# Kernel optimization log

Measured on AMD Instinct MI355X. Metric: run time of the kernel, lower is better.

## Reference

```python
import jax, jax.numpy as jnp
import numpy as np

B, N, F_IN = 32, 512, 64
HEADS = (8, 8)
HIDS = (64, 64)
EDGE_P = 0.05  # graph density
NEG_SLOPE = 0.2
NEG_INF = -1e20


def setup_inputs() -> dict:
    key = jax.random.key(0)
    ks = jax.random.split(key, 8)
    x = jax.random.normal(ks[0], (B, N, F_IN), dtype=jnp.float32)
    adj = (jax.random.uniform(ks[1], (B, N, N)) < EDGE_P).astype(jnp.float32)
    adj = jnp.maximum(adj, adj.transpose(0, 2, 1))  # symmetric adjacency
    # mask = (batch, row): every (b, n) pair gets the masked softmax
    b_idx = jnp.repeat(jnp.arange(B, dtype=jnp.int32), N)   # [B*N]
    r_idx = jnp.tile(jnp.arange(N, dtype=jnp.int32), B)     # [B*N]
    # layer 0: f_in=64 -> f_out=64, H=8 ; layer 1: f_in=64*8=512 -> f_out=64, H=8
    W0 = jax.random.normal(ks[2], (F_IN, HIDS[0]), dtype=jnp.float32) / jnp.sqrt(jnp.float32(F_IN))
    a_src0 = jax.random.normal(ks[3], (HIDS[0], HEADS[0]), dtype=jnp.float32) / jnp.sqrt(jnp.float32(HIDS[0]))
    a_dst0 = jax.random.normal(ks[4], (HIDS[0], HEADS[0]), dtype=jnp.float32) / jnp.sqrt(jnp.float32(HIDS[0]))
    f_in1 = HIDS[0] * HEADS[0]
    W1 = jax.random.normal(ks[5], (f_in1, HIDS[1]), dtype=jnp.float32) / jnp.sqrt(jnp.float32(f_in1))
    a_src1 = jax.random.normal(ks[6], (HIDS[1], HEADS[1]), dtype=jnp.float32) / jnp.sqrt(jnp.float32(HIDS[1]))
    a_dst1 = jax.random.normal(ks[7], (HIDS[1], HEADS[1]), dtype=jnp.float32) / jnp.sqrt(jnp.float32(HIDS[1]))
    return dict(x=x, adj=adj, b_idx=b_idx, r_idx=r_idx,
                W0=W0, a_src0=a_src0, a_dst0=a_dst0,
                W1=W1, a_src1=a_src1, a_dst1=a_dst1)


def _gat_layer(x, adj, b_idx, r_idx, W, a_src, a_dst):
    # x: [B,N,f_in], adj: [B,N,N] (diag already set), W: [f_in,F], a_*: [F,H]
    hp = x @ W                                        # [B,N,F]
    s = jnp.einsum('bnf,fh->bhn', hp, a_src)          # attn_src
    d = jnp.einsum('bnf,fh->bhn', hp, a_dst)          # attn_dst
    attn = s[:, :, :, None] + d[:, :, None, :]        # [B,H,N,N]
    attn = jnp.where(attn >= 0, attn, NEG_SLOPE * attn)  # leaky_relu(0.2)
    attn = jnp.where(adj[:, None, :, :] == 0, 0.0, attn)  # masked_fill(adj==0, 0)
    rows = attn[b_idx, :, r_idx, :]                   # [K,H,N]
    rows = jnp.where(rows == 0.0, NEG_INF, rows)
    rows = jax.nn.softmax(rows, axis=-1)
    attn = attn.at[b_idx, :, r_idx, :].set(rows)
    return jnp.einsum('bhij,bjf->bhif', attn, hp)     # [B,H,N,F]


def reference(x, adj, b_idx, r_idx, W0, a_src0, a_dst0, W1, a_src1, a_dst1):
    Bn, Nn = x.shape[:2]
    # torch mutates adj in place: adj[batch,row,row] = 1 (self loops)
    adj = adj.at[b_idx, r_idx, r_idx].set(1.0)
    o = _gat_layer(x, adj, b_idx, r_idx, W0, a_src0, a_dst0)      # [B,H,N,F0]
    x1 = jax.nn.elu(o.transpose(0, 2, 1, 3).reshape(Bn, Nn, -1))  # [B,N,H*F0]
    o2 = _gat_layer(x1, adj, b_idx, r_idx, W1, a_src1, a_dst1)    # [B,H,N,F1]
    return o2.mean(axis=1)                                        # [B,N,F1]
```

## Files before the change

### kernel.cpp

```cpp
#include <hip/hip_runtime.h>
#include <hip/hip_bf16.h>
#include <math.h>

#define BB 32
#define NN 512

typedef _Float16 f16x8 __attribute__((ext_vector_type(8)));
typedef __fp16  fp16x2 __attribute__((ext_vector_type(2)));
typedef float f32x4 __attribute__((ext_vector_type(4)));

#define MFMA16(a, b, c) __builtin_amdgcn_mfma_f32_16x16x32_f16(a, b, c, 0, 0, 0)

union AF { f16x8 v; unsigned int u[4]; };

__global__ __launch_bounds__(256) void k_wt_prep(
    const float* __restrict__ W0, _Float16* __restrict__ W0T,
    const float* __restrict__ W1, _Float16* __restrict__ W1T)
{
    int id = blockIdx.x * 256 + threadIdx.x;
    const float* W; _Float16* WT; int KT, task;
    if (id < 512) { W = W0; WT = W0T; KT = 64;  task = id; }
    else          { W = W1; WT = W1T; KT = 512; task = id - 512; }
    int n = task & 63, gabs = task >> 6;
    int c = gabs >> 3, g = gabs & 7;
    f16x8 hv;
#pragma unroll
    for (int e = 0; e < 8; ++e)
        hv[e] = (_Float16)W[(size_t)(gabs * 8 + e) * 64 + n];
    *(f16x8*)(WT + (size_t)n * KT + c * 64 + (g ^ (n & 7)) * 8) = hv;
}

__global__ __launch_bounds__(256) void k_maxd(
    const float* __restrict__ dTg, float* __restrict__ maxd)
{
    __shared__ float sm[4];
    int bh = blockIdx.x;
    int t = threadIdx.x, lane = t & 63, w = t >> 6;
    const float* p = dTg + (size_t)bh * NN;
    float m = fmaxf(p[t], p[t + 256]);
#pragma unroll
    for (int off = 32; off; off >>= 1) m = fmaxf(m, __shfl_xor(m, off));
    if (lane == 0) sm[w] = m;
    __syncthreads();
    if (t == 0) maxd[bh] = fmaxf(fmaxf(sm[0], sm[1]), fmaxf(sm[2], sm[3]));
}

static __device__ __forceinline__ void epi_sd_hpt(
    const float* ctile, const float* asd_f, int row0, int t,
    float* __restrict__ s, float* __restrict__ dTg, _Float16* __restrict__ hpT)
{
    int b = row0 >> 9, jb = row0 & 511;
    if (t < 128) {
        int rr = t >> 3, h = t & 7;
        float sv = 0.f, dv = 0.f;
#pragma unroll
        for (int f = 0; f < 64; ++f) {
            float hv = ctile[rr * 66 + f];
            sv = fmaf(hv, asd_f[f * 8 + h], sv);
            dv = fmaf(hv, asd_f[512 + f * 8 + h], dv);
        }
        s[((size_t)b * NN + jb + rr) * 8 + h] = sv;
        dTg[((size_t)b * 8 + h) * NN + jb + rr] = dv;
    } else {
        int t2 = t - 128;
        int f = t2 >> 1, jl = (t2 & 1) * 8;
        f16x8 hv;
#pragma unroll
        for (int e = 0; e < 8; ++e)
            hv[e] = (_Float16)ctile[(jl + e) * 66 + f];
        *(f16x8*)(hpT + ((size_t)b * 64 + f) * NN + jb + jl) = hv;
    }
}

__global__ __launch_bounds__(256) void k_gemm0(
    const float* __restrict__ x, const _Float16* __restrict__ W0T,
    const float* __restrict__ a_src, const float* __restrict__ a_dst,
    float* __restrict__ s, float* __restrict__ dTg, _Float16* __restrict__ hpT)
{
    __shared__ float ctile[16 * 66];
    __shared__ float asd_f[1024];
    int t = threadIdx.x, row0 = blockIdx.x * 16;
    int lane = t & 63, w = t >> 6, cn = lane & 15, rq = lane >> 4;

    ((float4*)asd_f)[t] = (t < 128) ? ((const float4*)a_src)[t]
                                    : ((const float4*)a_dst)[t - 128];
    f32x4 acc;
#pragma unroll
    for (int e = 0; e < 4; ++e) acc[e] = 0.f;
#pragma unroll
    for (int ks = 0; ks < 2; ++ks) {
        const float* xp = x + (size_t)(row0 + cn) * 64 + ks * 32 + rq * 8;
        float4 x0 = *(const float4*)xp, x1 = *(const float4*)(xp + 4);
        f16x8 ah = {(_Float16)x0.x, (_Float16)x0.y, (_Float16)x0.z, (_Float16)x0.w,
                    (_Float16)x1.x, (_Float16)x1.y, (_Float16)x1.z, (_Float16)x1.w};
        int nn = w * 16 + cn;
        f16x8 bh = *(const f16x8*)(W0T + (size_t)nn * 64 + (((ks * 4 + rq) ^ (nn & 7)) * 8));
        acc = MFMA16(ah, bh, acc);
    }
#pragma unroll
    for (int r = 0; r < 4; ++r)
        ctile[(rq * 4 + r) * 66 + w * 16 + cn] = acc[r];
    __syncthreads();
    epi_sd_hpt(ctile, asd_f, row0, t, s, dTg, hpT);
}

template<int MODE>
__global__ __launch_bounds__(256, 4) void k_attn_fused(
    const float* __restrict__ adj, const float* __restrict__ s,
    const float* __restrict__ dTg, const float* __restrict__ maxd,
    const _Float16* __restrict__ hpT,
    const _Float16* __restrict__ W1T,
    const float* __restrict__ a_src, const float* __restrict__ a_dst,
    float* __restrict__ s_out, float* __restrict__ dTg_out,
    _Float16* __restrict__ hpT_out, float* __restrict__ o_f)
{
    __shared__ __align__(16) char smem[32768];
    _Float16* hT = (_Float16*)smem;

    int blk = blockIdx.x;
    int vb = ((blk & 7) << 7) | (blk >> 3);
    int b = vb >> 5, i0 = (vb & 31) << 4;
    int row0 = vb * 16;
    int t = threadIdx.x, lane = t & 63, w = t >> 6;
    int cn = lane & 15, rq = lane >> 4;
    int h0 = 2 * w, h1 = h0 + 1;
    int myrow = i0 + cn;

    float sv0 = s[((size_t)b * NN + myrow) * 8 + h0];
    float sv1 = s[((size_t)b * NN + myrow) * 8 + h1];
    float M0 = fmaxf(sv0 + maxd[b * 8 + h0], 0.f);
    float M1 = fmaxf(sv1 + maxd[b * 8 + h1], 0.f);

    const float* arow = adj + ((size_t)b * NN + myrow) * NN;
    const float* dg0 = dTg + ((size_t)b * 8 + h0) * NN;
    const float* dg1 = dTg + ((size_t)b * 8 + h1) * NN;
    const _Float16* hb = hpT + (size_t)b * 64 * NN;

    int f0 = t >> 3, g0 = t & 7;
    int f1 = f0 + 32;
    int sw = ((g0 ^ (f0 & 7)) * 8);
    int sw0 = f0 * 64 + sw, sw1 = f1 * 64 + sw;

    f16x8 ones;
#pragma unroll
    for (int e = 0; e < 8; ++e) ones[e] = (_Float16)1.0f;

    f32x4 acc[2][4], accrs[2];
#pragma unroll
    for (int hh = 0; hh < 2; ++hh) {
#pragma unroll
        for (int e = 0; e < 4; ++e) accrs[hh][e] = 0.f;
#pragma unroll
        for (int ft = 0; ft < 4; ++ft)
#pragma unroll
            for (int e = 0; e < 4; ++e) acc[hh][ft][e] = 0.f;
    }

    uint4 rH0 = *(const uint4*)(hb + (size_t)f0 * 512 + g0 * 8);
    uint4 rH1 = *(const uint4*)(hb + (size_t)f1 * 512 + g0 * 8);

    for (int jcx = 0; jcx < 8; ++jcx) {
        int jc = jcx * 64;
        float aa[2][8], dd0[2][8], dd1[2][8];
#pragma unroll
        for (int ks = 0; ks < 2; ++ks) {
            int j0 = jc + ks * 32 + rq * 8;
            *(float4*)&aa[ks][0]  = *(const float4*)(arow + j0);
            *(float4*)&aa[ks][4]  = *(const float4*)(arow + j0 + 4);
            *(float4*)&dd0[ks][0] = *(const float4*)(dg0 + j0);
            *(float4*)&dd0[ks][4] = *(const float4*)(dg0 + j0 + 4);
            *(float4*)&dd1[ks][0] = *(const float4*)(dg1 + j0);
            *(float4*)&dd1[ks][4] = *(const float4*)(dg1 + j0 + 4);
        }
        *(uint4*)&hT[sw0] = rH0;
        *(uint4*)&hT[sw1] = rH1;
        __syncthreads();
        if (jcx < 7) {
            rH0 = *(const uint4*)(hb + (size_t)f0 * 512 + jc + 64 + g0 * 8);
            rH1 = *(const uint4*)(hb + (size_t)f1 * 512 + jc + 64 + g0 * 8);
        }
#pragma unroll
        for (int ks = 0; ks < 2; ++ks) {
            int j0 = jc + ks * 32 + rq * 8;
            int rel = myrow - j0;
            AF aA, aB;
#pragma unroll
            for (int e = 0; e < 8; e += 2) {
                float pA[2], pB[2];
#pragma unroll
                for (int q = 0; q < 2; ++q) {
                    int ee = e + q;
                    bool con = (aa[ks][ee] != 0.f) || (ee == rel);
                    float e0 = sv0 + dd0[ks][ee];
                    float l0 = fmaxf(e0, 0.2f * e0);
                    float p0 = __expf(l0 - M0);
                    pA[q] = (con && l0 != 0.f) ? p0 : 0.f;
                    float e1 = sv1 + dd1[ks][ee];
                    float l1 = fmaxf(e1, 0.2f * e1);
                    float p1 = __expf(l1 - M1);
                    pB[q] = (con && l1 != 0.f) ? p1 : 0.f;
                }
                fp16x2 ka = __builtin_amdgcn_cvt_pkrtz(pA[0], pA[1]);
                fp16x2 kb = __builtin_amdgcn_cvt_pkrtz(pB[0], pB[1]);
                aA.u[e >> 1] = __builtin_bit_cast(unsigned int, ka);
                aB.u[e >> 1] = __builtin_bit_cast(unsigned int, kb);
            }
            accrs[0] = MFMA16(aA.v, ones, accrs[0]);
            accrs[1] = MFMA16(aB.v, ones, accrs[1]);
#pragma unroll
            for (int ft = 0; ft < 4; ++ft) {
                int f = ft * 16 + cn;
                f16x8 bh = *(const f16x8*)&hT[f * 64 + (((ks * 4 + rq) ^ (f & 7)) * 8)];
                acc[0][ft] = MFMA16(aA.v, bh, acc[0][ft]);
                acc[1][ft] = MFMA16(aB.v, bh, acc[1][ft]);
            }
        }
        __syncthreads();
    }

    float invr[2][4];
#pragma unroll
    for (int hh = 0; hh < 2; ++hh)
#pragma unroll
        for (int r = 0; r < 4; ++r) invr[hh][r] = 1.0f / accrs[hh][r];

    if (MODE == 0) {
        _Float16* x1all = (_Float16*)(smem + 8192);
#pragma unroll
        for (int hh = 0; hh < 2; ++hh) {
            int h = h0 + hh;
#pragma unroll
            for (int ft = 0; ft < 4; ++ft)
#pragma unroll
                for (int r = 0; r < 4; ++r) {
                    int il = rq * 4 + r;
                    float v = acc[hh][ft][r] * invr[hh][r];
                    v = v > 0.f ? v : __expf(v) - 1.f;
                    int f = ft * 16 + cn;
                    x1all[h * 1024 + il * 64 + (((f >> 3) ^ (il & 7)) * 8) + (f & 7)] =
                        (_Float16)v;
                }
        }

        _Float16* Bst[2] = { (_Float16*)smem, (_Float16*)(smem + 24576) };
        {
#pragma unroll
            for (int u = 0; u < 2; ++u) {
                int idx = t + u * 256;
                *(uint4*)&Bst[0][idx * 8] =
                    *(const uint4*)(W1T + (size_t)(idx >> 3) * 512 + (idx & 7) * 8);
            }
        }
        f32x4 g1;
#pragma unroll
        for (int e = 0; e < 4; ++e) g1[e] = 0.f;
        uint4 rB0, rB1;
        for (int kc = 0; kc < 8; ++kc) {
            int cur = kc & 1;
            if (kc < 7) {
                rB0 = *(const uint4*)(W1T + (size_t)(t >> 3) * 512 + (kc + 1) * 64 + (t & 7) * 8);
                rB1 = *(const uint4*)(W1T + (size_t)((t + 256) >> 3) * 512 + (kc + 1) * 64 + (t & 7) * 8);
            }
            __syncthreads();
#pragma unroll
            for (int ks = 0; ks < 2; ++ks) {
                int pa = (((ks * 4 + rq) ^ (cn & 7)) * 8);
                f16x8 ah = *(const f16x8*)&x1all[kc * 1024 + cn * 64 + pa];
                int nn = w * 16 + cn;
                f16x8 bh = *(const f16x8*)&Bst[cur][nn * 64 + (((ks * 4 + rq) ^ (nn & 7)) * 8)];
                g1 = MFMA16(ah, bh, g1);
            }
            if (kc < 7) {
                *(uint4*)&Bst[cur ^ 1][t * 8] = rB0;
                *(uint4*)&Bst[cur ^ 1][(t + 256) * 8] = rB1;
            }
        }
        __syncthreads();
        float* ctile = (float*)(smem + 8192);
        float* asd_f = (float*)(smem + 16384);
#pragma unroll
        for (int r = 0; r < 4; ++r)
            ctile[(rq * 4 + r) * 66 + w * 16 + cn] = g1[r];
        ((float4*)asd_f)[t] = (t < 128) ? ((const float4*)a_src)[t]
                                        : ((const float4*)a_dst)[t - 128];
        __syncthreads();
        epi_sd_hpt(ctile, asd_f, row0, t, s_out, dTg_out, hpT_out);
    } else {
        float* red = (float*)smem;
#pragma unroll
        for (int ft = 0; ft < 4; ++ft)
#pragma unroll
            for (int r = 0; r < 4; ++r) {
                int il = rq * 4 + r;
                float v = acc[0][ft][r] * invr[0][r]
                        + acc[1][ft][r] * invr[1][r];
                red[(w * 16 + il) * 64 + ft * 16 + cn] = v;
            }
        __syncthreads();
#pragma unroll
        for (int u = 0; u < 4; ++u) {
            int idx = t + u * 256;
            int il = idx >> 6, f = idx & 63;
            float sum = red[il * 64 + f] + red[(16 + il) * 64 + f]
                      + red[(32 + il) * 64 + f] + red[(48 + il) * 64 + f];
            o_f[((size_t)b * NN + i0 + il) * 64 + f] = sum * 0.125f;
        }
    }
}

extern "C" void kernel_launch(void* const* d_in, const int* in_sizes, int n_in,
                              void* d_out, int out_size, void* d_ws, size_t ws_size,
                              hipStream_t stream) {
    const float* x      = (const float*)d_in[0];
    const float* adj    = (const float*)d_in[1];
    const float* W0     = (const float*)d_in[4];
    const float* a_src0 = (const float*)d_in[5];
    const float* a_dst0 = (const float*)d_in[6];
    const float* W1     = (const float*)d_in[7];
    const float* a_src1 = (const float*)d_in[8];
    const float* a_dst1 = (const float*)d_in[9];
    float* out = (float*)d_out;

    float* ws = (float*)d_ws;
    const size_t R = (size_t)BB * NN;
    float* s0    = ws;
    float* dTg0  = s0 + R * 8;
    float* s1    = dTg0 + (size_t)BB * 8 * NN;
    float* dTg1  = s1 + R * 8;
    float* maxd0 = dTg1 + (size_t)BB * 8 * NN;
    float* maxd1 = maxd0 + 256;
    _Float16* hp0T = (_Float16*)(maxd1 + 256);
    _Float16* hp1T = hp0T + (size_t)BB * 64 * NN;
    _Float16* W0T  = hp1T + (size_t)BB * 64 * NN;
    _Float16* W1T  = W0T + (size_t)64 * 64;

    k_wt_prep<<<18, 256, 0, stream>>>(W0, W0T, W1, W1T);
    k_gemm0<<<1024, 256, 0, stream>>>(x, W0T, a_src0, a_dst0, s0, dTg0, hp0T);
    k_maxd<<<256, 256, 0, stream>>>(dTg0, maxd0);
    k_attn_fused<0><<<1024, 256, 0, stream>>>(adj, s0, dTg0, maxd0, hp0T,
                                              W1T, a_src1, a_dst1,
                                              s1, dTg1, hp1T, nullptr);
    k_maxd<<<256, 256, 0, stream>>>(dTg1, maxd1);
    k_attn_fused<1><<<1024, 256, 0, stream>>>(adj, s1, dTg1, maxd1, hp1T,
                                              nullptr, nullptr, nullptr,
                                              nullptr, nullptr, nullptr, out);
}
```

Before: 164.4 us.

## Bitpack adjacency, factor softmax exponentials, and stage tiles via direct global-to-LDS loads

The adjacency matrix is packed into 64-bit ballot masks inside the first GEMM kernel, so the two attention passes read 1 bit instead of 4 bytes per edge. The exponential is factored into per-row and per-column terms: exp(d - max) and exp(0.2*(d - max)) are precomputed per column in the max kernel, leaving only a multiply per edge. The hpT and W1T tiles are double-buffered in LDS using global_load_lds, which removes the register round trip. The cost is extra E/Eb arrays that are read per element, and possible precision differences from the factored exponent.

After: 187.8 us. 14.2% more time.

```diff
diff --git a/kernel.cpp b/kernel.cpp
--- a/kernel.cpp
+++ b/kernel.cpp
@@ -12,6 +12,12 @@
 #define MFMA16(a, b, c) __builtin_amdgcn_mfma_f32_16x16x32_f16(a, b, c, 0, 0, 0)
 
 union AF { f16x8 v; unsigned int u[4]; };
+
+__device__ __forceinline__ void gload_lds16(const void* g, void* l) {
+    __builtin_amdgcn_global_load_lds(
+        (const __attribute__((address_space(1))) unsigned int*)g,
+        (__attribute__((address_space(3))) unsigned int*)l, 16, 0, 0);
+}
 
 __global__ __launch_bounds__(256) void k_wt_prep(
     const float* __restrict__ W0, _Float16* __restrict__ W0T,
@@ -31,18 +37,27 @@
 }
 
 __global__ __launch_bounds__(256) void k_maxd(
-    const float* __restrict__ dTg, float* __restrict__ maxd)
+    const float* __restrict__ dTg, float* __restrict__ maxd,
+    float* __restrict__ E, float* __restrict__ Eb)
 {
     __shared__ float sm[4];
     int bh = blockIdx.x;
     int t = threadIdx.x, lane = t & 63, w = t >> 6;
     const float* p = dTg + (size_t)bh * NN;
-    float m = fmaxf(p[t], p[t + 256]);
+    float d0 = p[t], d1 = p[t + 256];
+    float m = fmaxf(d0, d1);
 #pragma unroll
     for (int off = 32; off; off >>= 1) m = fmaxf(m, __shfl_xor(m, off));
     if (lane == 0) sm[w] = m;
     __syncthreads();
-    if (t == 0) maxd[bh] = fmaxf(fmaxf(sm[0], sm[1]), fmaxf(sm[2], sm[3]));
+    float mx = fmaxf(fmaxf(sm[0], sm[1]), fmaxf(sm[2], sm[3]));
+    if (t == 0) maxd[bh] = mx;
+    float* Ep  = E  + (size_t)bh * NN;
+    float* Ebp = Eb + (size_t)bh * NN;
+    Ep[t]        = __expf(d0 - mx);
+    Ep[t + 256]  = __expf(d1 - mx);
+    Ebp[t]       = __expf(0.2f * (d0 - mx));
+    Ebp[t + 256] = __expf(0.2f * (d1 - mx));
 }
 
 static __device__ __forceinline__ void epi_sd_hpt(
@@ -75,6 +90,7 @@
 __global__ __launch_bounds__(256) void k_gemm0(
     const float* __restrict__ x, const _Float16* __restrict__ W0T,
     const float* __restrict__ a_src, const float* __restrict__ a_dst,
+    const float* __restrict__ adj, unsigned long long* __restrict__ adjb,
     float* __restrict__ s, float* __restrict__ dTg, _Float16* __restrict__ hpT)
 {
     __shared__ float ctile[16 * 66];
@@ -102,12 +118,26 @@
         ctile[(rq * 4 + r) * 66 + w * 16 + cn] = acc[r];
     __syncthreads();
     epi_sd_hpt(ctile, asd_f, row0, t, s, dTg, hpT);
+
+#pragma unroll
+    for (int rl = 0; rl < 4; ++rl) {
+        int gi = row0 + w * 4 + rl;
+        int i = gi & (NN - 1);
+        const float* ap = adj + (size_t)gi * NN;
+#pragma unroll
+        for (int jc8 = 0; jc8 < 8; ++jc8) {
+            float v = ap[jc8 * 64 + lane];
+            unsigned long long m = __ballot((v != 0.f) || (jc8 * 64 + lane == i));
+            if (lane == 0) adjb[(size_t)gi * 8 + jc8] = m;
+        }
+    }
 }
 
 template<int MODE>
 __global__ __launch_bounds__(256, 4) void k_attn_fused(
-    const float* __restrict__ adj, const float* __restrict__ s,
+    const unsigned long long* __restrict__ adjb, const float* __restrict__ s,
     const float* __restrict__ dTg, const float* __restrict__ maxd,
+    const float* __restrict__ E, const float* __restrict__ Eb,
     const _Float16* __restrict__ hpT,
     const _Float16* __restrict__ W1T,
     const float* __restrict__ a_src, const float* __restrict__ a_dst,
@@ -115,7 +145,8 @@
     _Float16* __restrict__ hpT_out, float* __restrict__ o_f)
 {
     __shared__ __align__(16) char smem[32768];
-    _Float16* hT = (_Float16*)smem;
+    _Float16* hTd0 = (_Float16*)smem;
+    _Float16* hTd1 = (_Float16*)(smem + 8192);
 
     int blk = blockIdx.x;
     int vb = ((blk & 7) << 7) | (blk >> 3);
@@ -126,20 +157,33 @@
     int h0 = 2 * w, h1 = h0 + 1;
     int myrow = i0 + cn;
 
+    const _Float16* hb = hpT + (size_t)b * 64 * NN;
+
+    int f0 = t >> 3, g0 = t & 7;
+    const _Float16* src0 = hb + (size_t)f0 * NN + ((g0 ^ (f0 & 7)) * 8);
+    const _Float16* src1 = hb + (size_t)(f0 + 32) * NN + ((g0 ^ (f0 & 7)) * 8);
+    {
+        _Float16* db = hTd0 + (w << 9);
+        gload_lds16(src0, db);
+        gload_lds16(src1, db + 2048);
+    }
+
     float sv0 = s[((size_t)b * NN + myrow) * 8 + h0];
     float sv1 = s[((size_t)b * NN + myrow) * 8 + h1];
-    float M0 = fmaxf(sv0 + maxd[b * 8 + h0], 0.f);
-    float M1 = fmaxf(sv1 + maxd[b * 8 + h1], 0.f);
-
-    const float* arow = adj + ((size_t)b * NN + myrow) * NN;
-    const float* dg0 = dTg + ((size_t)b * 8 + h0) * NN;
-    const float* dg1 = dTg + ((size_t)b * 8 + h1) * NN;
-    const _Float16* hb = hpT + (size_t)b * 64 * NN;
-
-    int f0 = t >> 3, g0 = t & 7;
-    int f1 = f0 + 32;
-    int sw = ((g0 ^ (f0 & 7)) * 8);
-    int sw0 = f0 * 64 + sw, sw1 = f1 * 64 + sw;
+    float md0 = maxd[b * 8 + h0], md1 = maxd[b * 8 + h1];
+    float M0 = fmaxf(sv0 + md0, 0.f);
+    float M1 = fmaxf(sv1 + md1, 0.f);
+    float c00 = __expf(sv0 + md0 - M0), cb0 = __expf(0.2f * (sv0 + md0) - M0);
+    float c01 = __expf(sv1 + md1 - M1), cb1 = __expf(0.2f * (sv1 + md1) - M1);
+
+    const float* dg0  = dTg + ((size_t)b * 8 + h0) * NN;
+    const float* dg1  = dTg + ((size_t)b * 8 + h1) * NN;
+    const float* Er0  = E   + ((size_t)b * 8 + h0) * NN;
+    const float* Er1  = E   + ((size_t)b * 8 + h1) * NN;
+    const float* Ebr0 = Eb  + ((size_t)b * 8 + h0) * NN;
+    const float* Ebr1 = Eb  + ((size_t)b * 8 + h1) * NN;
+    const unsigned long long* abr = adjb + ((size_t)b * NN + myrow) * 8;
+    int rq8 = rq * 8;
 
     f16x8 ones;
 #pragma unroll
@@ -156,33 +200,37 @@
             for (int e = 0; e < 4; ++e) acc[hh][ft][e] = 0.f;
     }
 
-    uint4 rH0 = *(const uint4*)(hb + (size_t)f0 * 512 + g0 * 8);
-    uint4 rH1 = *(const uint4*)(hb + (size_t)f1 * 512 + g0 * 8);
-
+    unsigned long long mb = abr[0];
+    __syncthreads();
+
+#pragma unroll 2
     for (int jcx = 0; jcx < 8; ++jcx) {
         int jc = jcx * 64;
-        float aa[2][8], dd0[2][8], dd1[2][8];
+        const _Float16* hTc = (jcx & 1) ? hTd1 : hTd0;
+        if (jcx < 7) {
+            _Float16* db = ((jcx & 1) ? hTd0 : hTd1) + (w << 9);
+            gload_lds16(src0 + jc + 64, db);
+            gload_lds16(src1 + jc + 64, db + 2048);
+        }
+        unsigned long long mbn = (jcx < 7) ? abr[jcx + 1] : 0ull;
+        unsigned int ml = (unsigned int)mb, mhh = (unsigned int)(mb >> 32);
 #pragma unroll
         for (int ks = 0; ks < 2; ++ks) {
-            int j0 = jc + ks * 32 + rq * 8;
-            *(float4*)&aa[ks][0]  = *(const float4*)(arow + j0);
-            *(float4*)&aa[ks][4]  = *(const float4*)(arow + j0 + 4);
-            *(float4*)&dd0[ks][0] = *(const float4*)(dg0 + j0);
-            *(float4*)&dd0[ks][4] = *(const float4*)(dg0 + j0 + 4);
-            *(float4*)&dd1[ks][0] = *(const float4*)(dg1 + j0);
-            *(float4*)&dd1[ks][4] = *(const float4*)(dg1 + j0 + 4);
-        }
-        *(uint4*)&hT[sw0] = rH0;
-        *(uint4*)&hT[sw1] = rH1;
-        __syncthreads();
-        if (jcx < 7) {
-            rH0 = *(const uint4*)(hb + (size_t)f0 * 512 + jc + 64 + g0 * 8);
-            rH1 = *(const uint4*)(hb + (size_t)f1 * 512 + jc + 64 + g0 * 8);
-        }
-#pragma unroll
-        for (int ks = 0; ks < 2; ++ks) {
-            int j0 = jc + ks * 32 + rq * 8;
-            int rel = myrow - j0;
+            int j0 = jc + ks * 32 + rq8;
+            unsigned int mby = ((ks ? mhh : ml) >> rq8) & 0xffu;
+            float dd0[8], dd1[8], Ev0[8], Ev1[8], Eb0v[8], Eb1v[8];
+            *(float4*)&dd0[0]  = *(const float4*)(dg0 + j0);
+            *(float4*)&dd0[4]  = *(const float4*)(dg0 + j0 + 4);
+            *(float4*)&dd1[0]  = *(const float4*)(dg1 + j0);
+            *(float4*)&dd1[4]  = *(const float4*)(dg1 + j0 + 4);
+            *(float4*)&Ev0[0]  = *(const float4*)(Er0 + j0);
+            *(float4*)&Ev0[4]  = *(const float4*)(Er0 + j0 + 4);
+            *(float4*)&Ev1[0]  = *(const float4*)(Er1 + j0);
+            *(float4*)&Ev1[4]  = *(const float4*)(Er1 + j0 + 4);
+            *(float4*)&Eb0v[0] = *(const float4*)(Ebr0 + j0);
+            *(float4*)&Eb0v[4] = *(const float4*)(Ebr0 + j0 + 4);
+            *(float4*)&Eb1v[0] = *(const float4*)(Ebr1 + j0);
+            *(float4*)&Eb1v[4] = *(const float4*)(Ebr1 + j0 + 4);
             AF aA, aB;
 #pragma unroll
             for (int e = 0; e < 8; e += 2) {
@@ -190,15 +238,13 @@
 #pragma unroll
                 for (int q = 0; q < 2; ++q) {
                     int ee = e + q;
-                    bool con = (aa[ks][ee] != 0.f) || (ee == rel);
-                    float e0 = sv0 + dd0[ks][ee];
-                    float l0 = fmaxf(e0, 0.2f * e0);
-                    float p0 = __expf(l0 - M0);
-                    pA[q] = (con && l0 != 0.f) ? p0 : 0.f;
-                    float e1 = sv1 + dd1[ks][ee];
-                    float l1 = fmaxf(e1, 0.2f * e1);
-                    float p1 = __expf(l1 - M1);
-                    pB[q] = (con && l1 != 0.f) ? p1 : 0.f;
+                    bool con = (mby >> ee) & 1u;
+                    float e0 = sv0 + dd0[ee];
+                    float p0 = (e0 >= 0.f) ? c00 * Ev0[ee] : cb0 * Eb0v[ee];
+                    pA[q] = (con && e0 != 0.f) ? p0 : 0.f;
+                    float e1 = sv1 + dd1[ee];
+                    float p1 = (e1 >= 0.f) ? c01 * Ev1[ee] : cb1 * Eb1v[ee];
+                    pB[q] = (con && e1 != 0.f) ? p1 : 0.f;
                 }
                 fp16x2 ka = __builtin_amdgcn_cvt_pkrtz(pA[0], pA[1]);
                 fp16x2 kb = __builtin_amdgcn_cvt_pkrtz(pB[0], pB[1]);
@@ -210,11 +256,12 @@
 #pragma unroll
             for (int ft = 0; ft < 4; ++ft) {
                 int f = ft * 16 + cn;
-                f16x8 bh = *(const f16x8*)&hT[f * 64 + (((ks * 4 + rq) ^ (f & 7)) * 8)];
+                f16x8 bh = *(const f16x8*)&hTc[f * 64 + (((ks * 4 + rq) ^ (f & 7)) * 8)];
                 acc[0][ft] = MFMA16(aA.v, bh, acc[0][ft]);
                 acc[1][ft] = MFMA16(aB.v, bh, acc[1][ft]);
             }
         }
+        mb = mbn;
         __syncthreads();
     }
 
@@ -225,7 +272,15 @@
         for (int r = 0; r < 4; ++r) invr[hh][r] = 1.0f / accrs[hh][r];
 
     if (MODE == 0) {
-        _Float16* x1all = (_Float16*)(smem + 8192);
+        _Float16* Bst0 = (_Float16*)smem;
+        _Float16* Bst1 = (_Float16*)(smem + 8192);
+        const _Float16* wsrc = W1T + (size_t)(t >> 3) * 512 + ((t & 7) * 8);
+        {
+            _Float16* db = Bst0 + (w << 9);
+            gload_lds16(wsrc, db);
+            gload_lds16(wsrc + 32 * 512, db + 2048);
+        }
+        _Float16* x1all = (_Float16*)(smem + 16384);
 #pragma unroll
         for (int hh = 0; hh < 2; ++hh) {
             int h = h0 + hh;
@@ -241,43 +296,29 @@
                         (_Float16)v;
                 }
         }
-
-        _Float16* Bst[2] = { (_Float16*)smem, (_Float16*)(smem + 24576) };
-        {
-#pragma unroll
-            for (int u = 0; u < 2; ++u) {
-                int idx = t + u * 256;
-                *(uint4*)&Bst[0][idx * 8] =
-                    *(const uint4*)(W1T + (size_t)(idx >> 3) * 512 + (idx & 7) * 8);
-            }
-        }
+        __syncthreads();
         f32x4 g1;
 #pragma unroll
         for (int e = 0; e < 4; ++e) g1[e] = 0.f;
-        uint4 rB0, rB1;
         for (int kc = 0; kc < 8; ++kc) {
-            int cur = kc & 1;
+            const _Float16* Bc = (kc & 1) ? Bst1 : Bst0;
             if (kc < 7) {
-                rB0 = *(const uint4*)(W1T + (size_t)(t >> 3) * 512 + (kc + 1) * 64 + (t & 7) * 8);
-                rB1 = *(const uint4*)(W1T + (size_t)((t + 256) >> 3) * 512 + (kc + 1) * 64 + (t & 7) * 8);
-            }
-            __syncthreads();
+                _Float16* db = ((kc & 1) ? Bst0 : Bst1) + (w << 9);
+                gload_lds16(wsrc + (kc + 1) * 64, db);
+                gload_lds16(wsrc + 32 * 512 + (kc + 1) * 64, db + 2048);
+            }
 #pragma unroll
             for (int ks = 0; ks < 2; ++ks) {
                 int pa = (((ks * 4 + rq) ^ (cn & 7)) * 8);
                 f16x8 ah = *(const f16x8*)&x1all[kc * 1024 + cn * 64 + pa];
                 int nn = w * 16 + cn;
-                f16x8 bh = *(const f16x8*)&Bst[cur][nn * 64 + (((ks * 4 + rq) ^ (nn & 7)) * 8)];
+                f16x8 bh = *(const f16x8*)&Bc[nn * 64 + (((ks * 4 + rq) ^ (nn & 7)) * 8)];
                 g1 = MFMA16(ah, bh, g1);
             }
-            if (kc < 7) {
-                *(uint4*)&Bst[cur ^ 1][t * 8] = rB0;
-                *(uint4*)&Bst[cur ^ 1][(t + 256) * 8] = rB1;
-            }
-        }
-        __syncthreads();
-        float* ctile = (float*)(smem + 8192);
-        float* asd_f = (float*)(smem + 16384);
+            __syncthreads();
+        }
+        float* ctile = (float*)(smem + 16384);
+        float* asd_f = (float*)(smem + 24576);
 #pragma unroll
         for (int r = 0; r < 4; ++r)
             ctile[(rq * 4 + r) * 66 + w * 16 + cn] = g1[r];
@@ -323,25 +364,32 @@
 
     float* ws = (float*)d_ws;
     const size_t R = (size_t)BB * NN;
+    const size_t BHN = (size_t)BB * 8 * NN;
     float* s0    = ws;
     float* dTg0  = s0 + R * 8;
-    float* s1    = dTg0 + (size_t)BB * 8 * NN;
+    float* s1    = dTg0 + BHN;
     float* dTg1  = s1 + R * 8;
-    float* maxd0 = dTg1 + (size_t)BB * 8 * NN;
+    float* maxd0 = dTg1 + BHN;
     float* maxd1 = maxd0 + 256;
-    _Float16* hp0T = (_Float16*)(maxd1 + 256);
+    float* E0    = maxd1 + 256;
+    float* Eb0   = E0 + BHN;
+    float* E1    = Eb0 + BHN;
+    float* Eb1   = E1 + BHN;
+    _Float16* hp0T = (_Float16*)(Eb1 + BHN);
     _Float16* hp1T = hp0T + (size_t)BB * 64 * NN;
     _Float16* W0T  = hp1T + (size_t)BB * 64 * NN;
     _Float16* W1T  = W0T + (size_t)64 * 64;
+    unsigned long long* adjb = (unsigned long long*)(W1T + (size_t)64 * 512);
 
     k_wt_prep<<<18, 256, 0, stream>>>(W0, W0T, W1, W1T);
-    k_gemm0<<<1024, 256, 0, stream>>>(x, W0T, a_src0, a_dst0, s0, dTg0, hp0T);
-    k_maxd<<<256, 256, 0, stream>>>(dTg0, maxd0);
-    k_attn_fused<0><<<1024, 256, 0, stream>>>(adj, s0, dTg0, maxd0, hp0T,
-                                              W1T, a_src1, a_dst1,
+    k_gemm0<<<1024, 256, 0, stream>>>(x, W0T, a_src0, a_dst0, adj, adjb,
+                                      s0, dTg0, hp0T);
+    k_maxd<<<256, 256, 0, stream>>>(dTg0, maxd0, E0, Eb0);
+    k_attn_fused<0><<<1024, 256, 0, stream>>>(adjb, s0, dTg0, maxd0, E0, Eb0,
+                                              hp0T, W1T, a_src1, a_dst1,
                                               s1, dTg1, hp1T, nullptr);
-    k_maxd<<<256, 256, 0, stream>>>(dTg1, maxd1);
-    k_attn_fused<1><<<1024, 256, 0, stream>>>(adj, s1, dTg1, maxd1, hp1T,
-                                              nullptr, nullptr, nullptr,
+    k_maxd<<<256, 256, 0, stream>>>(dTg1, maxd1, E1, Eb1);
+    k_attn_fused<1><<<1024, 256, 0, stream>>>(adjb, s1, dTg1, maxd1, E1, Eb1,
+                                              hp1T, nullptr, nullptr, nullptr,
                                               nullptr, nullptr, nullptr, out);
 }
```
